# Performance work log

Measured on AMD Instinct MI355X. Metric: run time of the kernel, lower is better.

The kernel has to match this reference:

```python
import jax, jax.numpy as jnp
import numpy as np

N = 100000   # num entities
D = 128      # embed_dim
S = 8192     # num sparse nodes
P = 16       # paths per node (padded; invalid paths fully masked)
K = 16       # max endpoints per path (padded via mask)
H = D // 2   # MLP hidden


def setup_inputs() -> dict:
    key = jax.random.key(0)
    ks = jax.random.split(key, 6)
    entity_embeds = jax.random.normal(ks[0], (N, D), dtype=jnp.float32)
    sparse_ids = jnp.arange(S, dtype=jnp.int32)  # distinct sparse node ids
    endpoint_ids = jax.random.randint(ks[1], (S, P, K), 0, N, dtype=jnp.int32)
    endpoint_mask = jax.random.randint(ks[2], (S, P, K), 0, 2).astype(bool)
    W1 = jax.random.normal(ks[3], (D, H), dtype=jnp.float32) * (1.0 / np.sqrt(D))
    b1 = jnp.zeros((H,), dtype=jnp.float32)
    W2 = jax.random.normal(ks[4], (H, 1), dtype=jnp.float32) * (1.0 / np.sqrt(H))
    b2 = jnp.zeros((1,), dtype=jnp.float32)
    return {"entity_embeds": entity_embeds, "W1": W1, "b1": b1, "W2": W2,
            "b2": b2, "sparse_ids": sparse_ids, "endpoint_ids": endpoint_ids,
            "endpoint_mask": endpoint_mask}


def reference(entity_embeds, W1, b1, W2, b2, sparse_ids, endpoint_ids, endpoint_mask):
    # Gather endpoint embeddings reached by each (sparse node, path): [S,P,K,D]
    gathered = entity_embeds[endpoint_ids]
    m = endpoint_mask.astype(entity_embeds.dtype)[..., None]
    cnt = endpoint_mask.sum(-1)                                   # [S,P] endpoints per path
    agg = (gathered * m).sum(2) / jnp.maximum(cnt, 1)[..., None]  # masked mean [S,P,D]
    # path_weight_net: Linear -> ReLU -> Linear -> Sigmoid (scalar weight per path)
    h = jax.nn.relu(agg @ W1 + b1)                                # [S,P,H]
    w = jax.nn.sigmoid(h @ W2 + b2)                               # [S,P,1]
    valid = cnt > 0                                               # path had endpoints
    feat = jnp.where(valid[..., None], w * agg, 0.0)              # [S,P,D]
    nv = valid.sum(1)                                             # valid paths per node [S]
    node_feat = feat.sum(1) / jnp.maximum(nv, 1)[:, None]         # mean over valid paths
    node_feat = jnp.where((nv > 0)[:, None], node_feat, 0.0)
    # scatter per-sparse-node aggregate into [N,D] (others stay zero)
    remote = jnp.zeros_like(entity_embeds).at[sparse_ids].set(node_feat)
    return remote
```

## Files before the change

### kernel.cpp

```cpp
#include <hip/hip_runtime.h>
#include <hip/hip_bf16.h>

#define S_NODES 8192
#define P_PATHS 16
#define K_EP    16
#define D_DIM   128
#define H_DIM   64

typedef __bf16 bf16x8_t __attribute__((ext_vector_type(8)));
typedef float  f32x4_t  __attribute__((ext_vector_type(4)));

#define AGGF_STRIDE  132
#define AGGBF_STRIDE 136

__global__ __launch_bounds__(256)
void prep_w1_kernel(const float* __restrict__ W1, __bf16* __restrict__ w1t)
{
    const int idx = blockIdx.x * 256 + threadIdx.x;
    const int n = idx >> 7, d = idx & 127;
    w1t[idx] = (__bf16)W1[d * H_DIM + n];
}

__global__ __launch_bounds__(256, 8)
void PathGuidedAggregator_kernel(const float* __restrict__ ent,
                                 const float* __restrict__ b1,
                                 const float* __restrict__ W2,
                                 const float* __restrict__ b2,
                                 const int*   __restrict__ sids,
                                 const int*   __restrict__ eids,
                                 const void*  __restrict__ emask,
                                 const __bf16* __restrict__ w1t,
                                 float*       __restrict__ out)
{
    __shared__ float  aggf [P_PATHS][AGGF_STRIDE];
    __shared__ __bf16 aggbf[P_PATHS][AGGBF_STRIDE];
    __shared__ int    cnts[P_PATHS];
    __shared__ int    comp[4][4][K_EP];

    const int s    = blockIdx.x;
    const int tid  = threadIdx.x;
    const int wave = tid >> 6;
    const int lane = tid & 63;

    const unsigned int* mw = (const unsigned int*)emask;
    unsigned int probe = mw[lane];
    const bool floatMask = (__ballot(probe == 0x3F800000u) != 0ULL);
    const bool byteMask  = !floatMask && (__ballot(probe > 1u) != 0ULL);

    const int base = (s * P_PATHS + wave * 4) * K_EP;
    const int idv  = eids[base + lane];
    int mk;
    if (floatMask)     mk = (((const float*)emask)[base + lane] != 0.0f);
    else if (byteMask) mk = ((const unsigned char*)emask)[base + lane];
    else               mk = ((const int*)emask)[base + lane];
    const unsigned long long bits_all = __ballot(mk != 0);

    const int k16  = lane & 15;
    const int pgrp = lane >> 4;
    const unsigned int bits_p = (unsigned int)((bits_all >> (16 * pgrp)) & 0xFFFFu);

    comp[wave][pgrp][k16] = 0;
    if (mk) comp[wave][pgrp][__popc(bits_p & ((1u << k16) - 1u))] = idv;
    if (lane < 4) cnts[wave * 4 + lane] = __popc((unsigned int)((bits_all >> (16 * lane)) & 0xFFFFu));

    const int c0 = __popc((unsigned int)( bits_all        & 0xFFFFu));
    const int c1 = __popc((unsigned int)((bits_all >> 16) & 0xFFFFu));
    const int c2 = __popc((unsigned int)((bits_all >> 32) & 0xFFFFu));
    const int c3 = __popc((unsigned int)((bits_all >> 48) & 0xFFFFu));

    const int half = lane >> 5;
    const int col  = lane & 31;
    const float4* __restrict__ entc = (const float4*)ent + col;

    float4 acc0 = {0.f,0.f,0.f,0.f}, acc1 = acc0, acc2 = acc0, acc3 = acc0;
    #pragma unroll
    for (int u = 0; u < 8; ++u) {
        const int slot = 2 * u + half;
        const int id0 = comp[wave][0][slot];
        const int id1 = comp[wave][1][slot];
        const int id2 = comp[wave][2][slot];
        const int id3 = comp[wave][3][slot];
        if (slot < c0) { float4 v = entc[(size_t)id0 << 5]; acc0.x += v.x; acc0.y += v.y; acc0.z += v.z; acc0.w += v.w; }
        if (slot < c1) { float4 v = entc[(size_t)id1 << 5]; acc1.x += v.x; acc1.y += v.y; acc1.z += v.z; acc1.w += v.w; }
        if (slot < c2) { float4 v = entc[(size_t)id2 << 5]; acc2.x += v.x; acc2.y += v.y; acc2.z += v.z; acc2.w += v.w; }
        if (slot < c3) { float4 v = entc[(size_t)id3 << 5]; acc3.x += v.x; acc3.y += v.y; acc3.z += v.z; acc3.w += v.w; }
    }

    #pragma unroll
    for (int i = 0; i < 4; ++i) {
        float4 a = (i == 0) ? acc0 : (i == 1) ? acc1 : (i == 2) ? acc2 : acc3;
        const int cnt = (i == 0) ? c0 : (i == 1) ? c1 : (i == 2) ? c2 : c3;
        a.x += __shfl_xor(a.x, 32); a.y += __shfl_xor(a.y, 32);
        a.z += __shfl_xor(a.z, 32); a.w += __shfl_xor(a.w, 32);
        const float inv = 1.0f / (float)(cnt > 1 ? cnt : 1);
        a.x *= inv; a.y *= inv; a.z *= inv; a.w *= inv;
        if (half == 0) {
            const int p = wave * 4 + i;
            *(float4*)&aggf[p][col * 4] = a;
            union { __bf16 h[4]; uint2 u2; } pk;
            pk.h[0] = (__bf16)a.x; pk.h[1] = (__bf16)a.y;
            pk.h[2] = (__bf16)a.z; pk.h[3] = (__bf16)a.w;
            *(uint2*)&aggbf[p][col * 4] = pk.u2;
        }
    }
    __syncthreads();

    if (wave != 0) return;

    const int m    = lane & 15;
    const int quad = lane >> 4;

    bf16x8_t afr[4];
    #pragma unroll
    for (int st = 0; st < 4; ++st)
        afr[st] = *(const bf16x8_t*)&aggbf[m][st * 32 + quad * 8];

    float xp[4] = {0.f, 0.f, 0.f, 0.f};
    #pragma unroll
    for (int t = 0; t < 4; ++t) {
        const int n = t * 16 + m;
        const float b1v = b1[n];
        f32x4_t acc = {b1v, b1v, b1v, b1v};
        const __bf16* bp = w1t + n * D_DIM + quad * 8;
        #pragma unroll
        for (int st = 0; st < 4; ++st) {
            bf16x8_t bfr = *(const bf16x8_t*)(bp + st * 32);
            acc = __builtin_amdgcn_mfma_f32_16x16x32_bf16(afr[st], bfr, acc, 0, 0, 0);
        }
        const float w2v = W2[n];
        #pragma unroll
        for (int r = 0; r < 4; ++r) {
            float h = acc[r] > 0.f ? acc[r] : 0.f;
            xp[r] += h * w2v;
        }
    }
    #pragma unroll
    for (int off = 1; off < 16; off <<= 1) {
        #pragma unroll
        for (int r = 0; r < 4; ++r) xp[r] += __shfl_xor(xp[r], off);
    }

    int myc[4]; int localv = 0;
    #pragma unroll
    for (int r = 0; r < 4; ++r) { myc[r] = cnts[quad * 4 + r]; localv += (myc[r] > 0); }
    int nv = localv + __shfl_xor(localv, 16);
    nv += __shfl_xor(nv, 32);
    const float invnv = 1.0f / (float)(nv > 1 ? nv : 1);
    const float b2v = b2[0];

    float wv[4];
    #pragma unroll
    for (int r = 0; r < 4; ++r) {
        float x = xp[r] + b2v;
        float w = 1.0f / (1.0f + __expf(-x));
        wv[r] = (myc[r] > 0) ? w * invnv : 0.f;
    }

    float fx = 0.f, fy = 0.f;
    #pragma unroll
    for (int p = 0; p < P_PATHS; ++p) {
        float wp = __shfl(wv[p & 3], (p >> 2) << 4);
        float2 a = *(const float2*)&aggf[p][2 * lane];
        fx += wp * a.x; fy += wp * a.y;
    }
    const int row = sids[s];
    *(float2*)&out[(size_t)row * D_DIM + 2 * lane] = make_float2(fx, fy);
}

extern "C" void kernel_launch(void* const* d_in, const int* in_sizes, int n_in,
                              void* d_out, int out_size, void* d_ws, size_t ws_size,
                              hipStream_t stream)
{
    const float* ent  = (const float*)d_in[0];
    const float* W1   = (const float*)d_in[1];
    const float* b1   = (const float*)d_in[2];
    const float* W2   = (const float*)d_in[3];
    const float* b2   = (const float*)d_in[4];
    const int*   sids = (const int*)d_in[5];
    const int*   eids = (const int*)d_in[6];
    const void*  emsk = (const void*)d_in[7];
    float* out = (float*)d_out;
    __bf16* w1t_ws = (__bf16*)d_ws;

    hipMemsetAsync(d_out, 0, (size_t)out_size * sizeof(float), stream);
    prep_w1_kernel<<<32, 256, 0, stream>>>(W1, w1t_ws);
    PathGuidedAggregator_kernel<<<S_NODES, 256, 0, stream>>>(ent, b1, W2, b2, sids, eids, emsk,
                                                             (const __bf16*)w1t_ws, out);
}
```

Measured before the change: 188.7 us.

## Gather endpoint embeddings from a bf16 copy of the entity table

Adds a prep kernel that converts the full entity table to bf16 in workspace, and switches the per-path gather to read 16-byte bf16 chunks with a reworked lane mapping (16 lanes per row, 4 slots in parallel) that unpacks into fp32 accumulators. This aims to halve the bytes moved by the random gathers, which dominate the kernel. The price is an extra pass over the 51 MB table each call, plus reduced precision on the aggregated embeddings. Launch bounds drop from 8 to 7 waves per SIMD, and the old fp32 path is kept as a fallback when the workspace is too small.

Measured after the change: 211.2 us. +12.0%, slower.

```diff
diff --git a/kernel.cpp b/kernel.cpp
--- a/kernel.cpp
+++ b/kernel.cpp
@@ -21,16 +21,37 @@
     w1t[idx] = (__bf16)W1[d * H_DIM + n];
 }
 
-__global__ __launch_bounds__(256, 8)
-void PathGuidedAggregator_kernel(const float* __restrict__ ent,
-                                 const float* __restrict__ b1,
-                                 const float* __restrict__ W2,
-                                 const float* __restrict__ b2,
-                                 const int*   __restrict__ sids,
-                                 const int*   __restrict__ eids,
-                                 const void*  __restrict__ emask,
+__global__ __launch_bounds__(256)
+void prep_ent_kernel(const float* __restrict__ ent, __bf16* __restrict__ entbf, int n4)
+{
+    const int i = blockIdx.x * 256 + threadIdx.x;
+    if (i >= n4) return;
+    float4 v = ((const float4*)ent)[i];
+    union { __bf16 h[4]; uint2 u; } pk;
+    pk.h[0] = (__bf16)v.x; pk.h[1] = (__bf16)v.y;
+    pk.h[2] = (__bf16)v.z; pk.h[3] = (__bf16)v.w;
+    ((uint2*)entbf)[i] = pk.u;
+}
+
+#define ACC8(acc, v) {                                                          \
+    unsigned w0 = (v).x, w1 = (v).y, w2 = (v).z, w3 = (v).w;                    \
+    acc[0] += __uint_as_float(w0 << 16); acc[1] += __uint_as_float(w0 & 0xffff0000u); \
+    acc[2] += __uint_as_float(w1 << 16); acc[3] += __uint_as_float(w1 & 0xffff0000u); \
+    acc[4] += __uint_as_float(w2 << 16); acc[5] += __uint_as_float(w2 & 0xffff0000u); \
+    acc[6] += __uint_as_float(w3 << 16); acc[7] += __uint_as_float(w3 & 0xffff0000u); }
+
+template<bool USE_BF16>
+__global__ __launch_bounds__(256, 7)
+void PathGuidedAggregator_kernel(const float*  __restrict__ ent,
+                                 const __bf16* __restrict__ entbf,
+                                 const float*  __restrict__ b1,
+                                 const float*  __restrict__ W2,
+                                 const float*  __restrict__ b2,
+                                 const int*    __restrict__ sids,
+                                 const int*    __restrict__ eids,
+                                 const void*   __restrict__ emask,
                                  const __bf16* __restrict__ w1t,
-                                 float*       __restrict__ out)
+                                 float*        __restrict__ out)
 {
     __shared__ float  aggf [P_PATHS][AGGF_STRIDE];
     __shared__ __bf16 aggbf[P_PATHS][AGGBF_STRIDE];
@@ -63,44 +84,94 @@
     if (mk) comp[wave][pgrp][__popc(bits_p & ((1u << k16) - 1u))] = idv;
     if (lane < 4) cnts[wave * 4 + lane] = __popc((unsigned int)((bits_all >> (16 * lane)) & 0xFFFFu));
 
-    const int c0 = __popc((unsigned int)( bits_all        & 0xFFFFu));
-    const int c1 = __popc((unsigned int)((bits_all >> 16) & 0xFFFFu));
-    const int c2 = __popc((unsigned int)((bits_all >> 32) & 0xFFFFu));
-    const int c3 = __popc((unsigned int)((bits_all >> 48) & 0xFFFFu));
-
-    const int half = lane >> 5;
-    const int col  = lane & 31;
-    const float4* __restrict__ entc = (const float4*)ent + col;
-
-    float4 acc0 = {0.f,0.f,0.f,0.f}, acc1 = acc0, acc2 = acc0, acc3 = acc0;
-    #pragma unroll
-    for (int u = 0; u < 8; ++u) {
-        const int slot = 2 * u + half;
-        const int id0 = comp[wave][0][slot];
-        const int id1 = comp[wave][1][slot];
-        const int id2 = comp[wave][2][slot];
-        const int id3 = comp[wave][3][slot];
-        if (slot < c0) { float4 v = entc[(size_t)id0 << 5]; acc0.x += v.x; acc0.y += v.y; acc0.z += v.z; acc0.w += v.w; }
-        if (slot < c1) { float4 v = entc[(size_t)id1 << 5]; acc1.x += v.x; acc1.y += v.y; acc1.z += v.z; acc1.w += v.w; }
-        if (slot < c2) { float4 v = entc[(size_t)id2 << 5]; acc2.x += v.x; acc2.y += v.y; acc2.z += v.z; acc2.w += v.w; }
-        if (slot < c3) { float4 v = entc[(size_t)id3 << 5]; acc3.x += v.x; acc3.y += v.y; acc3.z += v.z; acc3.w += v.w; }
-    }
-
-    #pragma unroll
-    for (int i = 0; i < 4; ++i) {
-        float4 a = (i == 0) ? acc0 : (i == 1) ? acc1 : (i == 2) ? acc2 : acc3;
-        const int cnt = (i == 0) ? c0 : (i == 1) ? c1 : (i == 2) ? c2 : c3;
-        a.x += __shfl_xor(a.x, 32); a.y += __shfl_xor(a.y, 32);
-        a.z += __shfl_xor(a.z, 32); a.w += __shfl_xor(a.w, 32);
-        const float inv = 1.0f / (float)(cnt > 1 ? cnt : 1);
-        a.x *= inv; a.y *= inv; a.z *= inv; a.w *= inv;
-        if (half == 0) {
-            const int p = wave * 4 + i;
-            *(float4*)&aggf[p][col * 4] = a;
-            union { __bf16 h[4]; uint2 u2; } pk;
-            pk.h[0] = (__bf16)a.x; pk.h[1] = (__bf16)a.y;
-            pk.h[2] = (__bf16)a.z; pk.h[3] = (__bf16)a.w;
-            *(uint2*)&aggbf[p][col * 4] = pk.u2;
+    const int carr0 = __popc((unsigned int)( bits_all        & 0xFFFFu));
+    const int carr1 = __popc((unsigned int)((bits_all >> 16) & 0xFFFFu));
+    const int carr2 = __popc((unsigned int)((bits_all >> 32) & 0xFFFFu));
+    const int carr3 = __popc((unsigned int)((bits_all >> 48) & 0xFFFFu));
+
+    if constexpr (USE_BF16) {
+        const int q   = lane >> 4;
+        const int c16 = lane & 15;
+        const uint4* __restrict__ entb = (const uint4*)entbf;
+        const int cl[4] = {carr0, carr1, carr2, carr3};
+        #pragma unroll
+        for (int pr = 0; pr < 2; ++pr) {
+            const int pA = pr * 2, pB = pr * 2 + 1;
+            const int cA = cl[pA], cB = cl[pB];
+            uint4 vA[4], vB[4];
+            bool  gA[4], gB[4];
+            #pragma unroll
+            for (int u = 0; u < 4; ++u) {
+                const int slot = u * 4 + q;
+                const int ida = comp[wave][pA][slot];
+                const int idb = comp[wave][pB][slot];
+                gA[u] = slot < cA; gB[u] = slot < cB;
+                if (gA[u]) vA[u] = entb[(size_t)ida * 16 + c16];
+                if (gB[u]) vB[u] = entb[(size_t)idb * 16 + c16];
+            }
+            float aA[8] = {0,0,0,0,0,0,0,0}, aB[8] = {0,0,0,0,0,0,0,0};
+            #pragma unroll
+            for (int u = 0; u < 4; ++u) {
+                if (gA[u]) ACC8(aA, vA[u]);
+                if (gB[u]) ACC8(aB, vB[u]);
+            }
+            #pragma unroll
+            for (int j = 0; j < 8; ++j) {
+                aA[j] += __shfl_xor(aA[j], 16); aA[j] += __shfl_xor(aA[j], 32);
+                aB[j] += __shfl_xor(aB[j], 16); aB[j] += __shfl_xor(aB[j], 32);
+            }
+            const float iA = 1.0f / (float)(cA > 1 ? cA : 1);
+            const float iB = 1.0f / (float)(cB > 1 ? cB : 1);
+            if (lane < 16) {
+                #pragma unroll
+                for (int j = 0; j < 8; ++j) { aA[j] *= iA; aB[j] *= iB; }
+                const int ppA = wave * 4 + pA, ppB = wave * 4 + pB;
+                *(float4*)&aggf[ppA][c16 * 8]     = make_float4(aA[0], aA[1], aA[2], aA[3]);
+                *(float4*)&aggf[ppA][c16 * 8 + 4] = make_float4(aA[4], aA[5], aA[6], aA[7]);
+                *(float4*)&aggf[ppB][c16 * 8]     = make_float4(aB[0], aB[1], aB[2], aB[3]);
+                *(float4*)&aggf[ppB][c16 * 8 + 4] = make_float4(aB[4], aB[5], aB[6], aB[7]);
+                union { __bf16 h[8]; uint4 u4; } pk;
+                #pragma unroll
+                for (int j = 0; j < 8; ++j) pk.h[j] = (__bf16)aA[j];
+                *(uint4*)&aggbf[ppA][c16 * 8] = pk.u4;
+                #pragma unroll
+                for (int j = 0; j < 8; ++j) pk.h[j] = (__bf16)aB[j];
+                *(uint4*)&aggbf[ppB][c16 * 8] = pk.u4;
+            }
+        }
+    } else {
+        const int half = lane >> 5;
+        const int col  = lane & 31;
+        const float4* __restrict__ entc = (const float4*)ent + col;
+        float4 acc0 = {0.f,0.f,0.f,0.f}, acc1 = acc0, acc2 = acc0, acc3 = acc0;
+        #pragma unroll
+        for (int u = 0; u < 8; ++u) {
+            const int slot = 2 * u + half;
+            const int id0 = comp[wave][0][slot];
+            const int id1 = comp[wave][1][slot];
+            const int id2 = comp[wave][2][slot];
+            const int id3 = comp[wave][3][slot];
+            if (slot < carr0) { float4 v = entc[(size_t)id0 << 5]; acc0.x += v.x; acc0.y += v.y; acc0.z += v.z; acc0.w += v.w; }
+            if (slot < carr1) { float4 v = entc[(size_t)id1 << 5]; acc1.x += v.x; acc1.y += v.y; acc1.z += v.z; acc1.w += v.w; }
+            if (slot < carr2) { float4 v = entc[(size_t)id2 << 5]; acc2.x += v.x; acc2.y += v.y; acc2.z += v.z; acc2.w += v.w; }
+            if (slot < carr3) { float4 v = entc[(size_t)id3 << 5]; acc3.x += v.x; acc3.y += v.y; acc3.z += v.z; acc3.w += v.w; }
+        }
+        #pragma unroll
+        for (int i = 0; i < 4; ++i) {
+            float4 a = (i == 0) ? acc0 : (i == 1) ? acc1 : (i == 2) ? acc2 : acc3;
+            const int cnt = (i == 0) ? carr0 : (i == 1) ? carr1 : (i == 2) ? carr2 : carr3;
+            a.x += __shfl_xor(a.x, 32); a.y += __shfl_xor(a.y, 32);
+            a.z += __shfl_xor(a.z, 32); a.w += __shfl_xor(a.w, 32);
+            const float inv = 1.0f / (float)(cnt > 1 ? cnt : 1);
+            a.x *= inv; a.y *= inv; a.z *= inv; a.w *= inv;
+            if (half == 0) {
+                const int p = wave * 4 + i;
+                *(float4*)&aggf[p][col * 4] = a;
+                union { __bf16 h[4]; uint2 u2; } pk;
+                pk.h[0] = (__bf16)a.x; pk.h[1] = (__bf16)a.y;
+                pk.h[2] = (__bf16)a.z; pk.h[3] = (__bf16)a.w;
+                *(uint2*)&aggbf[p][col * 4] = pk.u2;
+            }
         }
     }
     __syncthreads();
@@ -180,10 +251,21 @@
     const int*   eids = (const int*)d_in[6];
     const void*  emsk = (const void*)d_in[7];
     float* out = (float*)d_out;
+
+    const int ND = in_sizes[0];
     __bf16* w1t_ws = (__bf16*)d_ws;
+    __bf16* entbf  = (__bf16*)((char*)d_ws + 16384);
+    const bool useBf16 = (ws_size >= 16384 + (size_t)ND * 2) && ((ND & 3) == 0);
 
     hipMemsetAsync(d_out, 0, (size_t)out_size * sizeof(float), stream);
     prep_w1_kernel<<<32, 256, 0, stream>>>(W1, w1t_ws);
-    PathGuidedAggregator_kernel<<<S_NODES, 256, 0, stream>>>(ent, b1, W2, b2, sids, eids, emsk,
-                                                             (const __bf16*)w1t_ws, out);
-}
+    if (useBf16) {
+        const int n4 = ND >> 2;
+        prep_ent_kernel<<<(n4 + 255) / 256, 256, 0, stream>>>(ent, entbf, n4);
+        PathGuidedAggregator_kernel<true><<<S_NODES, 256, 0, stream>>>(
+            ent, (const __bf16*)entbf, b1, W2, b2, sids, eids, emsk, (const __bf16*)w1t_ws, out);
+    } else {
+        PathGuidedAggregator_kernel<false><<<S_NODES, 256, 0, stream>>>(
+            ent, (const __bf16*)entbf, b1, W2, b2, sids, eids, emsk, (const __bf16*)w1t_ws, out);
+    }
+}
```

## Gather entity embeddings from a bf16 copy to halve gather traffic

Applied to the files above, without the earlier changes.

Adds a prep kernel that converts the whole entity table to bf16 in workspace each call. The aggregation then gathers 16-byte bf16 rows of 8 elements per lane and accumulates them in fp32, with a new lane layout of 4 slots by 16 columns and an xor-shuffle reduction. This targets random-gather bandwidth, since each gathered row shrinks from 512 to 256 bytes. In exchange, the full table (about 51 MB read, 25 MB written) is converted every call, endpoint values are rounded to bf16 before averaging, and the occupancy hint drops from 8 to 6.

Measured after the change: 177.8 us. 5.8% less time.

```diff
diff --git a/kernel.cpp b/kernel.cpp
--- a/kernel.cpp
+++ b/kernel.cpp
@@ -21,16 +21,46 @@
     w1t[idx] = (__bf16)W1[d * H_DIM + n];
 }
 
-__global__ __launch_bounds__(256, 8)
-void PathGuidedAggregator_kernel(const float* __restrict__ ent,
-                                 const float* __restrict__ b1,
-                                 const float* __restrict__ W2,
-                                 const float* __restrict__ b2,
-                                 const int*   __restrict__ sids,
-                                 const int*   __restrict__ eids,
-                                 const void*  __restrict__ emask,
+__global__ __launch_bounds__(256)
+void prep_ent_kernel(const float* __restrict__ ent, __bf16* __restrict__ entbf, int n4)
+{
+    const int i = blockIdx.x * 256 + threadIdx.x;
+    if (i >= n4) return;
+    float4 v = ((const float4*)ent)[i];
+    union { __bf16 h[4]; uint2 u; } pk;
+    pk.h[0] = (__bf16)v.x; pk.h[1] = (__bf16)v.y;
+    pk.h[2] = (__bf16)v.z; pk.h[3] = (__bf16)v.w;
+    ((uint2*)entbf)[i] = pk.u;
+}
+
+__device__ __forceinline__ void acc_row(float4& lo, float4& hi, uint4 r)
+{
+    lo.x += __uint_as_float(r.x << 16); lo.y += __uint_as_float(r.x & 0xffff0000u);
+    lo.z += __uint_as_float(r.y << 16); lo.w += __uint_as_float(r.y & 0xffff0000u);
+    hi.x += __uint_as_float(r.z << 16); hi.y += __uint_as_float(r.z & 0xffff0000u);
+    hi.z += __uint_as_float(r.w << 16); hi.w += __uint_as_float(r.w & 0xffff0000u);
+}
+
+__device__ __forceinline__ void merge_xor(float4& v)
+{
+    v.x += __shfl_xor(v.x, 16); v.y += __shfl_xor(v.y, 16);
+    v.z += __shfl_xor(v.z, 16); v.w += __shfl_xor(v.w, 16);
+    v.x += __shfl_xor(v.x, 32); v.y += __shfl_xor(v.y, 32);
+    v.z += __shfl_xor(v.z, 32); v.w += __shfl_xor(v.w, 32);
+}
+
+template<bool USE_BF16>
+__global__ __launch_bounds__(256, 6)
+void PathGuidedAggregator_kernel(const float*  __restrict__ ent,
+                                 const __bf16* __restrict__ entbf,
+                                 const float*  __restrict__ b1,
+                                 const float*  __restrict__ W2,
+                                 const float*  __restrict__ b2,
+                                 const int*    __restrict__ sids,
+                                 const int*    __restrict__ eids,
+                                 const void*   __restrict__ emask,
                                  const __bf16* __restrict__ w1t,
-                                 float*       __restrict__ out)
+                                 float*        __restrict__ out)
 {
     __shared__ float  aggf [P_PATHS][AGGF_STRIDE];
     __shared__ __bf16 aggbf[P_PATHS][AGGBF_STRIDE];
@@ -68,39 +98,75 @@
     const int c2 = __popc((unsigned int)((bits_all >> 32) & 0xFFFFu));
     const int c3 = __popc((unsigned int)((bits_all >> 48) & 0xFFFFu));
 
-    const int half = lane >> 5;
-    const int col  = lane & 31;
-    const float4* __restrict__ entc = (const float4*)ent + col;
-
-    float4 acc0 = {0.f,0.f,0.f,0.f}, acc1 = acc0, acc2 = acc0, acc3 = acc0;
-    #pragma unroll
-    for (int u = 0; u < 8; ++u) {
-        const int slot = 2 * u + half;
-        const int id0 = comp[wave][0][slot];
-        const int id1 = comp[wave][1][slot];
-        const int id2 = comp[wave][2][slot];
-        const int id3 = comp[wave][3][slot];
-        if (slot < c0) { float4 v = entc[(size_t)id0 << 5]; acc0.x += v.x; acc0.y += v.y; acc0.z += v.z; acc0.w += v.w; }
-        if (slot < c1) { float4 v = entc[(size_t)id1 << 5]; acc1.x += v.x; acc1.y += v.y; acc1.z += v.z; acc1.w += v.w; }
-        if (slot < c2) { float4 v = entc[(size_t)id2 << 5]; acc2.x += v.x; acc2.y += v.y; acc2.z += v.z; acc2.w += v.w; }
-        if (slot < c3) { float4 v = entc[(size_t)id3 << 5]; acc3.x += v.x; acc3.y += v.y; acc3.z += v.z; acc3.w += v.w; }
-    }
-
-    #pragma unroll
-    for (int i = 0; i < 4; ++i) {
-        float4 a = (i == 0) ? acc0 : (i == 1) ? acc1 : (i == 2) ? acc2 : acc3;
-        const int cnt = (i == 0) ? c0 : (i == 1) ? c1 : (i == 2) ? c2 : c3;
-        a.x += __shfl_xor(a.x, 32); a.y += __shfl_xor(a.y, 32);
-        a.z += __shfl_xor(a.z, 32); a.w += __shfl_xor(a.w, 32);
-        const float inv = 1.0f / (float)(cnt > 1 ? cnt : 1);
-        a.x *= inv; a.y *= inv; a.z *= inv; a.w *= inv;
-        if (half == 0) {
-            const int p = wave * 4 + i;
-            *(float4*)&aggf[p][col * 4] = a;
-            union { __bf16 h[4]; uint2 u2; } pk;
-            pk.h[0] = (__bf16)a.x; pk.h[1] = (__bf16)a.y;
-            pk.h[2] = (__bf16)a.z; pk.h[3] = (__bf16)a.w;
-            *(uint2*)&aggbf[p][col * 4] = pk.u2;
+    const int q   = lane >> 4;
+    const int c16 = lane & 15;
+
+    if constexpr (USE_BF16) {
+        const uint4* __restrict__ entb = (const uint4*)entbf + c16;
+        float4 l0 = {0,0,0,0}, h0 = l0, l1 = l0, h1 = l0, l2 = l0, h2 = l0, l3 = l0, h3 = l0;
+        #pragma unroll
+        for (int u = 0; u < 4; ++u) {
+            const int slot = q + 4 * u;
+            const bool g0 = slot < c0, g1 = slot < c1, g2 = slot < c2, g3 = slot < c3;
+            uint4 r0, r1, r2, r3;
+            if (g0) r0 = entb[(size_t)comp[wave][0][slot] * 16];
+            if (g1) r1 = entb[(size_t)comp[wave][1][slot] * 16];
+            if (g2) r2 = entb[(size_t)comp[wave][2][slot] * 16];
+            if (g3) r3 = entb[(size_t)comp[wave][3][slot] * 16];
+            if (g0) acc_row(l0, h0, r0);
+            if (g1) acc_row(l1, h1, r1);
+            if (g2) acc_row(l2, h2, r2);
+            if (g3) acc_row(l3, h3, r3);
+        }
+        merge_xor(l0); merge_xor(h0); merge_xor(l1); merge_xor(h1);
+        merge_xor(l2); merge_xor(h2); merge_xor(l3); merge_xor(h3);
+
+        const int   cq   = (q == 0) ? c0 : (q == 1) ? c1 : (q == 2) ? c2 : c3;
+        const float invq = 1.0f / (float)(cq > 1 ? cq : 1);
+        float4 lo = (q == 0) ? l0 : (q == 1) ? l1 : (q == 2) ? l2 : l3;
+        float4 hi = (q == 0) ? h0 : (q == 1) ? h1 : (q == 2) ? h2 : h3;
+        lo.x *= invq; lo.y *= invq; lo.z *= invq; lo.w *= invq;
+        hi.x *= invq; hi.y *= invq; hi.z *= invq; hi.w *= invq;
+        const int pw = wave * 4 + q;
+        *(float4*)&aggf[pw][c16 * 8]     = lo;
+        *(float4*)&aggf[pw][c16 * 8 + 4] = hi;
+        union { __bf16 h[8]; uint4 u4; } pk;
+        pk.h[0] = (__bf16)lo.x; pk.h[1] = (__bf16)lo.y; pk.h[2] = (__bf16)lo.z; pk.h[3] = (__bf16)lo.w;
+        pk.h[4] = (__bf16)hi.x; pk.h[5] = (__bf16)hi.y; pk.h[6] = (__bf16)hi.z; pk.h[7] = (__bf16)hi.w;
+        *(uint4*)&aggbf[pw][c16 * 8] = pk.u4;
+    } else {
+        const int half = lane >> 5;
+        const int col  = lane & 31;
+        const float4* __restrict__ entc = (const float4*)ent + col;
+        float4 acc0 = {0.f,0.f,0.f,0.f}, acc1 = acc0, acc2 = acc0, acc3 = acc0;
+        #pragma unroll
+        for (int u = 0; u < 8; ++u) {
+            const int slot = 2 * u + half;
+            const int id0 = comp[wave][0][slot];
+            const int id1 = comp[wave][1][slot];
+            const int id2 = comp[wave][2][slot];
+            const int id3 = comp[wave][3][slot];
+            if (slot < c0) { float4 v = entc[(size_t)id0 << 5]; acc0.x += v.x; acc0.y += v.y; acc0.z += v.z; acc0.w += v.w; }
+            if (slot < c1) { float4 v = entc[(size_t)id1 << 5]; acc1.x += v.x; acc1.y += v.y; acc1.z += v.z; acc1.w += v.w; }
+            if (slot < c2) { float4 v = entc[(size_t)id2 << 5]; acc2.x += v.x; acc2.y += v.y; acc2.z += v.z; acc2.w += v.w; }
+            if (slot < c3) { float4 v = entc[(size_t)id3 << 5]; acc3.x += v.x; acc3.y += v.y; acc3.z += v.z; acc3.w += v.w; }
+        }
+        #pragma unroll
+        for (int i = 0; i < 4; ++i) {
+            float4 a = (i == 0) ? acc0 : (i == 1) ? acc1 : (i == 2) ? acc2 : acc3;
+            const int cnt = (i == 0) ? c0 : (i == 1) ? c1 : (i == 2) ? c2 : c3;
+            a.x += __shfl_xor(a.x, 32); a.y += __shfl_xor(a.y, 32);
+            a.z += __shfl_xor(a.z, 32); a.w += __shfl_xor(a.w, 32);
+            const float inv = 1.0f / (float)(cnt > 1 ? cnt : 1);
+            a.x *= inv; a.y *= inv; a.z *= inv; a.w *= inv;
+            if (half == 0) {
+                const int p = wave * 4 + i;
+                *(float4*)&aggf[p][col * 4] = a;
+                union { __bf16 h[4]; uint2 u2; } pk;
+                pk.h[0] = (__bf16)a.x; pk.h[1] = (__bf16)a.y;
+                pk.h[2] = (__bf16)a.z; pk.h[3] = (__bf16)a.w;
+                *(uint2*)&aggbf[p][col * 4] = pk.u2;
+            }
         }
     }
     __syncthreads();
@@ -180,10 +246,21 @@
     const int*   eids = (const int*)d_in[6];
     const void*  emsk = (const void*)d_in[7];
     float* out = (float*)d_out;
+
+    const int ND = in_sizes[0];
     __bf16* w1t_ws = (__bf16*)d_ws;
+    __bf16* entbf  = (__bf16*)((char*)d_ws + 16384);
+    const bool useBf16 = (ws_size >= 16384 + (size_t)ND * 2) && ((ND & 3) == 0);
 
     hipMemsetAsync(d_out, 0, (size_t)out_size * sizeof(float), stream);
     prep_w1_kernel<<<32, 256, 0, stream>>>(W1, w1t_ws);
-    PathGuidedAggregator_kernel<<<S_NODES, 256, 0, stream>>>(ent, b1, W2, b2, sids, eids, emsk,
-                                                             (const __bf16*)w1t_ws, out);
-}
+    if (useBf16) {
+        const int n4 = ND >> 2;
+        prep_ent_kernel<<<(n4 + 255) / 256, 256, 0, stream>>>(ent, entbf, n4);
+        PathGuidedAggregator_kernel<true><<<S_NODES, 256, 0, stream>>>(
+            ent, (const __bf16*)entbf, b1, W2, b2, sids, eids, emsk, (const __bf16*)w1t_ws, out);
+    } else {
+        PathGuidedAggregator_kernel<false><<<S_NODES, 256, 0, stream>>>(
+            ent, (const __bf16*)entbf, b1, W2, b2, sids, eids, emsk, (const __bf16*)w1t_ws, out);
+    }
+}
```
